# Optimization experiments

Measured on AMD Instinct MI355X. Metric: run time of the kernel, lower is better.

The kernel has to match this reference:

```python
import jax, jax.numpy as jnp
import numpy as np

NUM_NODES = 50000
NUM_EDGES = 1600000
IN_DIM = 128
OUT_DIM = 128
BATCH = 2


def setup_inputs() -> dict:
    key = jax.random.key(0)
    k1, k2, k3 = jax.random.split(key, 3)
    inputs = jax.random.normal(k1, (BATCH, NUM_NODES, IN_DIM), dtype=jnp.float32)
    W = jax.random.normal(k2, (IN_DIM, OUT_DIM), dtype=jnp.float32) * 0.02
    bias = jnp.zeros((1, 1, OUT_DIM), dtype=jnp.float32)
    adjacency_list = jax.random.randint(k3, (NUM_EDGES, 2), 0, NUM_NODES, dtype=jnp.int32)
    return {"inputs": inputs, "W": W, "bias": bias, "adjacency_list": adjacency_list}


def reference(inputs, W, bias, adjacency_list):
    # inputs: (B, N, Din); adjacency_list: (E, 2) with [:,0]=src, [:,1]=dst
    N = inputs.shape[1]
    src = adjacency_list[:, 0]
    dst = adjacency_list[:, 1]
    # symmetric-normalization weights, as computed in __init__
    deg = jnp.bincount(src, length=N)                      # (N,)
    node_w = jnp.sqrt(1.0 / (deg.astype(inputs.dtype) + 1.0))  # (N,)
    edge_w = node_w[src] * node_w[dst]                     # (E,)
    # dense projection (no activation: activation=None)
    x = jnp.einsum('bnd,do->bno', inputs, W)               # (B, N, Dout)
    # gather by edge source, scale by edge weight
    gathered = x[:, src, :] * edge_w[None, :, None]        # (B, E, Dout)
    # scatter-add into destination nodes (unsorted_segment_sum)
    agg = jnp.zeros_like(x).at[:, dst, :].add(gathered)    # (B, N, Dout)
    # self-loop term + aggregated neighbors + bias
    out = (node_w ** 2)[None, :, None] * x + agg + bias
    return out
```

## Files before the change

### kernel.cpp

```cpp
#include <hip/hip_runtime.h>
#include <hip/hip_bf16.h>


#define NN 50000
#define EE 1600000
#define DD 128
#define BB 2
#define NB 128
#define CHUNK 12500
#define HS 50000
#define HW4 (HS / 4)

typedef __attribute__((ext_vector_type(8))) short short8;
typedef __attribute__((ext_vector_type(8))) unsigned short ushort8v;
typedef __attribute__((ext_vector_type(4))) float floatx4;

__device__ inline unsigned short f2bf(float f) {
    unsigned u = __float_as_uint(f);
    unsigned r = u + 0x7fffu + ((u >> 16) & 1u);
    return (unsigned short)(r >> 16);
}
__device__ inline float bf2f(unsigned short h) {
    return __uint_as_float(((unsigned)h) << 16);
}

__global__ __launch_bounds__(1024) void phist_kernel(const int4* __restrict__ adj2,
                                                     unsigned int* __restrict__ histD32,
                                                     unsigned int* __restrict__ histS32,
                                                     unsigned char* __restrict__ rank) {
    __shared__ unsigned int h[HW4];
    int b = blockIdx.x;
    int p0 = b * (CHUNK / 2);

    for (int i = threadIdx.x; i < HW4; i += 1024) h[i] = 0;
    __syncthreads();
    if (blockIdx.y == 0) {
        for (int i = threadIdx.x; i < CHUNK / 2; i += 1024) {
            int4 two = adj2[p0 + i];
            unsigned ka = (unsigned)two.y, kb = (unsigned)two.w;
            unsigned sha = (ka & 3u) << 3, shb = (kb & 3u) << 3;
            unsigned olda = atomicAdd(&h[ka >> 2], 1u << sha);
            unsigned oldb = atomicAdd(&h[kb >> 2], 1u << shb);
            unsigned r0 = (olda >> sha) & 0xffu;
            unsigned r1 = (oldb >> shb) & 0xffu;
            int e = b * CHUNK + 2 * i;
            *(unsigned short*)(rank + e) = (unsigned short)(r0 | (r1 << 8));
        }
        __syncthreads();
        for (int i = threadIdx.x; i < HW4; i += 1024) histD32[(size_t)b * HW4 + i] = h[i];
    } else {
        for (int i = threadIdx.x; i < CHUNK / 2; i += 1024) {
            int4 two = adj2[p0 + i];
            unsigned ka = (unsigned)two.x, kb = (unsigned)two.z;
            atomicAdd(&h[ka >> 2], 1u << ((ka & 3u) << 3));
            atomicAdd(&h[kb >> 2], 1u << ((kb & 3u) << 3));
        }
        __syncthreads();
        for (int i = threadIdx.x; i < HW4; i += 1024) histS32[(size_t)b * HW4 + i] = h[i];
    }
}

__global__ __launch_bounds__(256) void reduce_hist_kernel(unsigned char* __restrict__ histD,
                                                          const unsigned char* __restrict__ histS,
                                                          unsigned char* __restrict__ deg8,
                                                          float* __restrict__ node_w,
                                                          int* __restrict__ blocksum) {
    int k = blockIdx.x * 256 + threadIdx.x;
    unsigned run = 0;
    if (k < NN) {
#pragma unroll 8
        for (int b = 0; b < NB; ++b) {
            size_t idx = (size_t)b * HS + k;
            unsigned c = histD[idx];
            histD[idx] = (unsigned char)run;
            run += c;
        }
        deg8[k] = (unsigned char)run;

        unsigned s = 0;
#pragma unroll 8
        for (int b = 0; b < NB; ++b) s += histS[(size_t)b * HS + k];
        node_w[k] = rsqrtf((float)s + 1.0f);
    }
    __shared__ int red[256];
    red[threadIdx.x] = (int)run;
    __syncthreads();
    for (int s2 = 128; s2 > 0; s2 >>= 1) {
        if (threadIdx.x < s2) red[threadIdx.x] += red[threadIdx.x + s2];
        __syncthreads();
    }
    if (threadIdx.x == 0) blocksum[blockIdx.x] = red[0];
}

__global__ __launch_bounds__(256) void offsets_kernel(const unsigned char* __restrict__ deg8,
                                                      const int* __restrict__ blocksum,
                                                      int* __restrict__ offsets) {
    __shared__ int base_s;
    __shared__ int s[256];
    int bid = blockIdx.x;
    if (threadIdx.x < 64) {
        int v = 0;
        for (int i = threadIdx.x; i < bid; i += 64) v += blocksum[i];
#pragma unroll
        for (int o = 32; o > 0; o >>= 1) v += __shfl_down(v, o);
        if (threadIdx.x == 0) base_s = v;
    }
    int t = bid * 256 + threadIdx.x;
    int d = (t < NN) ? deg8[t] : 0;
    s[threadIdx.x] = d;
    __syncthreads();
    for (int off = 1; off < 256; off <<= 1) {
        int v = (threadIdx.x >= off) ? s[threadIdx.x - off] : 0;
        __syncthreads();
        s[threadIdx.x] += v;
        __syncthreads();
    }
    if (t < NN) offsets[t] = base_s + s[threadIdx.x] - d;
}

__global__ __launch_bounds__(256) void scatter_kernel(const int4* __restrict__ adj2,
                                                      const unsigned short* __restrict__ rank16,
                                                      const unsigned char* __restrict__ histD,
                                                      const int* __restrict__ offsets,
                                                      unsigned short* __restrict__ csr_src) {
    int i = blockIdx.x * blockDim.x + threadIdx.x;
    int4 two = adj2[i];
    unsigned rr = rank16[i];
    int e = 2 * i;
    int b = e / CHUNK;
    int posA = offsets[two.y] + (int)histD[(size_t)b * HS + two.y] + (int)(rr & 0xffu);
    int posB = offsets[two.w] + (int)histD[(size_t)b * HS + two.w] + (int)(rr >> 8);
    csr_src[posA] = (unsigned short)two.x;
    csr_src[posB] = (unsigned short)two.z;
}

#define WT_STRIDE 136
__global__ __launch_bounds__(1024) void gemm_mfma_kernel(const float* __restrict__ in,
                                                         const float* __restrict__ W,
                                                         const float* __restrict__ node_w,
                                                         unsigned short* __restrict__ y,
                                                         int total_rows) {
    __shared__ unsigned short wt[128 * WT_STRIDE];
    for (int i = threadIdx.x; i < 128 * 128; i += 1024) {
        int d = i >> 7, o = i & 127;
        wt[o * WT_STRIDE + d] = f2bf(W[i]);
    }
    __syncthreads();

    int wave = threadIdx.x >> 6;
    int lane = threadIdx.x & 63;
    int m = lane & 15;
    int quad = lane >> 4;
    int rt = (blockIdx.x * 16 + wave) * 16;
    if (rt >= total_rows) return;

    short8 a[4];
    const float* arow = in + (size_t)(rt + m) * 128;
#pragma unroll
    for (int kt = 0; kt < 4; ++kt) {
        int k0 = kt * 32 + quad * 8;
        float4 f0 = *(const float4*)(arow + k0);
        float4 f1 = *(const float4*)(arow + k0 + 4);
        short8 av;
        av[0] = (short)f2bf(f0.x); av[1] = (short)f2bf(f0.y);
        av[2] = (short)f2bf(f0.z); av[3] = (short)f2bf(f0.w);
        av[4] = (short)f2bf(f1.x); av[5] = (short)f2bf(f1.y);
        av[6] = (short)f2bf(f1.z); av[7] = (short)f2bf(f1.w);
        a[kt] = av;
    }

    float nw[4];
#pragma unroll
    for (int r = 0; r < 4; ++r) {
        int row = rt + quad * 4 + r;
        int n = row - (row >= NN ? NN : 0);
        nw[r] = node_w[n];
    }

#pragma unroll
    for (int ct = 0; ct < 8; ++ct) {
        floatx4 acc = {0.f, 0.f, 0.f, 0.f};
#pragma unroll
        for (int kt = 0; kt < 4; ++kt) {
            const short8* bp =
                (const short8*)&wt[(ct * 16 + m) * WT_STRIDE + kt * 32 + quad * 8];
            acc = __builtin_amdgcn_mfma_f32_16x16x32_bf16(a[kt], *bp, acc, 0, 0, 0);
        }
        int col = ct * 16 + m;
#pragma unroll
        for (int r = 0; r < 4; ++r) {
            int row = rt + quad * 4 + r;
            y[(size_t)row * 128 + col] = f2bf(nw[r] * acc[r]);
        }
    }
}

__global__ __launch_bounds__(256) void aggregate_kernel(
    const unsigned short* __restrict__ yb, const unsigned short* __restrict__ csr_src,
    const int* __restrict__ offsets, const unsigned char* __restrict__ deg8,
    const float* __restrict__ node_w, const float* __restrict__ bias,
    float* __restrict__ out) {
    int wave = threadIdx.x >> 6;
    int lane = threadIdx.x & 63;
    unsigned blk = blockIdx.x;
    int xcd = (int)(blk & 7u);
    int bg = xcd >> 2;
    int nbid = (int)(blk >> 3) * 4 + (xcd & 3);
    int n = nbid * 4 + wave;

    int g = lane >> 4;
    int c8 = lane & 15;
    int c16 = c8 * 16;
    const char* ybase = (const char*)yb + (size_t)bg * (NN * 128 * 2);

    int start = offsets[n];
    int cnt = deg8[n];

    float acc[8];
#pragma unroll
    for (int k = 0; k < 8; ++k) acc[k] = 0.f;

    for (int base = 0; base < cnt; base += 64) {
        int mm = cnt - base; if (mm > 64) mm = 64;
        int v = (lane < mm) ? (int)csr_src[start + base + lane] : 0x7fffffff;
#pragma unroll
        for (int k = 2; k <= 64; k <<= 1) {
#pragma unroll
            for (int j = k >> 1; j > 0; j >>= 1) {
                int other = __shfl_xor(v, j);
                bool lower = (lane & j) == 0;
                bool up = (lane & k) == 0;
                int mn = other < v ? other : v;
                int mx = other < v ? v : other;
                v = up ? (lower ? mn : mx) : (lower ? mx : mn);
            }
        }
        int sv = v << 8;
        int j = 0;
        for (; j + 16 <= mm; j += 16) {
            int o0 = __shfl(sv, j + g) + c16;
            int o1 = __shfl(sv, j + 4 + g) + c16;
            int o2 = __shfl(sv, j + 8 + g) + c16;
            int o3 = __shfl(sv, j + 12 + g) + c16;
            ushort8v ld0 = *(const ushort8v*)(ybase + (unsigned)o0);
            ushort8v ld1 = *(const ushort8v*)(ybase + (unsigned)o1);
            ushort8v ld2 = *(const ushort8v*)(ybase + (unsigned)o2);
            ushort8v ld3 = *(const ushort8v*)(ybase + (unsigned)o3);
#pragma unroll
            for (int k = 0; k < 8; ++k) acc[k] += bf2f((unsigned short)ld0[k]);
#pragma unroll
            for (int k = 0; k < 8; ++k) acc[k] += bf2f((unsigned short)ld1[k]);
#pragma unroll
            for (int k = 0; k < 8; ++k) acc[k] += bf2f((unsigned short)ld2[k]);
#pragma unroll
            for (int k = 0; k < 8; ++k) acc[k] += bf2f((unsigned short)ld3[k]);
        }
        for (; j + 8 <= mm; j += 8) {
            int o0 = __shfl(sv, j + g) + c16;
            int o1 = __shfl(sv, j + 4 + g) + c16;
            ushort8v ld0 = *(const ushort8v*)(ybase + (unsigned)o0);
            ushort8v ld1 = *(const ushort8v*)(ybase + (unsigned)o1);
#pragma unroll
            for (int k = 0; k < 8; ++k) acc[k] += bf2f((unsigned short)ld0[k]);
#pragma unroll
            for (int k = 0; k < 8; ++k) acc[k] += bf2f((unsigned short)ld1[k]);
        }
        if (j < mm) {
            int i0 = j + g, i1 = j + 4 + g;
            int o0 = __shfl(sv, i0 < mm ? i0 : 0) + c16;
            int o1 = __shfl(sv, i1 < mm ? i1 : 0) + c16;
            if (i0 < mm) {
                ushort8v ld0 = *(const ushort8v*)(ybase + (unsigned)o0);
#pragma unroll
                for (int k = 0; k < 8; ++k) acc[k] += bf2f((unsigned short)ld0[k]);
            }
            if (i1 < mm) {
                ushort8v ld1 = *(const ushort8v*)(ybase + (unsigned)o1);
#pragma unroll
                for (int k = 0; k < 8; ++k) acc[k] += bf2f((unsigned short)ld1[k]);
            }
        }
    }

#pragma unroll
    for (int k = 0; k < 8; ++k) {
        acc[k] += __shfl_xor(acc[k], 16);
        acc[k] += __shfl_xor(acc[k], 32);
    }

    if (g == 0) {
        float nw = node_w[n];
        const unsigned short* ys = yb + (size_t)bg * (NN * 128) + (size_t)n * 128 + c8 * 8;
        ushort8v yv = *(const ushort8v*)ys;
        floatx4 o0, o1;
        const float* bp = bias + c8 * 8;
        o0.x = nw * (acc[0] + bf2f((unsigned short)yv[0])) + bp[0];
        o0.y = nw * (acc[1] + bf2f((unsigned short)yv[1])) + bp[1];
        o0.z = nw * (acc[2] + bf2f((unsigned short)yv[2])) + bp[2];
        o0.w = nw * (acc[3] + bf2f((unsigned short)yv[3])) + bp[3];
        o1.x = nw * (acc[4] + bf2f((unsigned short)yv[4])) + bp[4];
        o1.y = nw * (acc[5] + bf2f((unsigned short)yv[5])) + bp[5];
        o1.z = nw * (acc[6] + bf2f((unsigned short)yv[6])) + bp[6];
        o1.w = nw * (acc[7] + bf2f((unsigned short)yv[7])) + bp[7];
        float* op = out + ((size_t)bg * NN + n) * 128 + c8 * 8;
        __builtin_nontemporal_store(o0, (floatx4*)op);
        __builtin_nontemporal_store(o1, (floatx4*)(op + 4));
    }
}

extern "C" void kernel_launch(void* const* d_in, const int* in_sizes, int n_in,
                              void* d_out, int out_size, void* d_ws, size_t ws_size,
                              hipStream_t stream) {
    const float* inputs = (const float*)d_in[0];
    const float* W      = (const float*)d_in[1];
    const float* bias   = (const float*)d_in[2];
    const int*   adj    = (const int*)d_in[3];
    float* out = (float*)d_out;

    const int total_rows = BB * NN;

    char* ws = (char*)d_ws;
    size_t off = 0;
    unsigned short* y = (unsigned short*)(ws + off);
    off += (size_t)BB * NN * DD * sizeof(unsigned short);
    unsigned char* histD = (unsigned char*)(ws + off);
    off += (size_t)NB * HS;
    unsigned char* histS = (unsigned char*)(ws + off);
    off += (size_t)NB * HS;
    unsigned short* csr_src = (unsigned short*)histS;
    unsigned char* rank = (unsigned char*)(ws + off);
    off += (size_t)EE;
    unsigned char* deg8 = (unsigned char*)(ws + off);
    off += (size_t)((NN + 255) & ~255);
    float* node_w = (float*)(ws + off);  off += (size_t)NN * sizeof(float);
    int* offsets = (int*)(ws + off);     off += (size_t)NN * sizeof(int);
    int* blocksum = (int*)(ws + off);    off += 256 * sizeof(int);

    dim3 hgrid(NB, 2);
    phist_kernel<<<hgrid, 1024, 0, stream>>>((const int4*)adj, (unsigned int*)histD,
                                             (unsigned int*)histS, rank);
    reduce_hist_kernel<<<(NN + 255) / 256, 256, 0, stream>>>(histD, histS, deg8, node_w,
                                                             blocksum);
    offsets_kernel<<<(NN + 255) / 256, 256, 0, stream>>>(deg8, blocksum, offsets);
    scatter_kernel<<<EE / 2 / 256, 256, 0, stream>>>((const int4*)adj,
                                                     (const unsigned short*)rank, histD, offsets,
                                                     csr_src);
    gemm_mfma_kernel<<<(total_rows + 255) / 256, 1024, 0, stream>>>(inputs, W, node_w, y,
                                                                    total_rows);
    aggregate_kernel<<<NN / 4 * BB, 256, 0, stream>>>(y, csr_src, offsets, deg8, node_w, bias,
                                                      out);
}
```

Before: 265.5 us.

## Fuse CSR scatter and MFMA GEMM into one interleaved kernel launch

Merges the independent edge-scatter and projection GEMM kernels into a single launch. Block indices are interleaved so that every third block does GEMM work and the other two do scatter work, letting the memory-bound scatter overlap with the compute-bound GEMM and removing one launch and its serialization point. Scatter blocks now use 1024 threads and still allocate the GEMM's static shared memory, which can lower occupancy for them. The aggregate kernel also gets an occupancy hint in its launch bounds and readfirstlane on the per-node start and count values to keep them in scalar registers.

```diff
diff --git a/kernel.cpp b/kernel.cpp
--- a/kernel.cpp
+++ b/kernel.cpp
@@ -10,6 +10,9 @@
 #define CHUNK 12500
 #define HS 50000
 #define HW4 (HS / 4)
+
+#define GEMM_BLOCKS 391
+#define SCAT_BLOCKS 782
 
 typedef __attribute__((ext_vector_type(8))) short short8;
 typedef __attribute__((ext_vector_type(8))) unsigned short ushort8v;
@@ -118,28 +121,29 @@
     if (t < NN) offsets[t] = base_s + s[threadIdx.x] - d;
 }
 
-__global__ __launch_bounds__(256) void scatter_kernel(const int4* __restrict__ adj2,
-                                                      const unsigned short* __restrict__ rank16,
-                                                      const unsigned char* __restrict__ histD,
-                                                      const int* __restrict__ offsets,
-                                                      unsigned short* __restrict__ csr_src) {
-    int i = blockIdx.x * blockDim.x + threadIdx.x;
-    int4 two = adj2[i];
-    unsigned rr = rank16[i];
-    int e = 2 * i;
-    int b = e / CHUNK;
-    int posA = offsets[two.y] + (int)histD[(size_t)b * HS + two.y] + (int)(rr & 0xffu);
-    int posB = offsets[two.w] + (int)histD[(size_t)b * HS + two.w] + (int)(rr >> 8);
-    csr_src[posA] = (unsigned short)two.x;
-    csr_src[posB] = (unsigned short)two.z;
-}
-
 #define WT_STRIDE 136
-__global__ __launch_bounds__(1024) void gemm_mfma_kernel(const float* __restrict__ in,
-                                                         const float* __restrict__ W,
-                                                         const float* __restrict__ node_w,
-                                                         unsigned short* __restrict__ y,
-                                                         int total_rows) {
+__global__ __launch_bounds__(1024) void scatter_gemm_kernel(
+    const int4* __restrict__ adj2, const unsigned short* __restrict__ rank16,
+    const unsigned char* __restrict__ histD, const int* __restrict__ offsets,
+    unsigned short* __restrict__ csr_src,
+    const float* __restrict__ in, const float* __restrict__ W,
+    const float* __restrict__ node_w, unsigned short* __restrict__ y) {
+    int bx = blockIdx.x;
+    int gq = bx / 3, r = bx - 3 * gq;
+    if (r != 0) {
+        int i = (2 * gq + r - 1) * 1024 + threadIdx.x;
+        if (i < EE / 2) {
+            int4 two = adj2[i];
+            unsigned rr = rank16[i];
+            int e = 2 * i;
+            int b = e / CHUNK;
+            int posA = offsets[two.y] + (int)histD[(size_t)b * HS + two.y] + (int)(rr & 0xffu);
+            int posB = offsets[two.w] + (int)histD[(size_t)b * HS + two.w] + (int)(rr >> 8);
+            csr_src[posA] = (unsigned short)two.x;
+            csr_src[posB] = (unsigned short)two.z;
+        }
+        return;
+    }
     __shared__ unsigned short wt[128 * WT_STRIDE];
     for (int i = threadIdx.x; i < 128 * 128; i += 1024) {
         int d = i >> 7, o = i & 127;
@@ -151,8 +155,8 @@
     int lane = threadIdx.x & 63;
     int m = lane & 15;
     int quad = lane >> 4;
-    int rt = (blockIdx.x * 16 + wave) * 16;
-    if (rt >= total_rows) return;
+    int rt = (gq * 16 + wave) * 16;
+    if (rt >= BB * NN) return;
 
     short8 a[4];
     const float* arow = in + (size_t)(rt + m) * 128;
@@ -171,10 +175,10 @@
 
     float nw[4];
 #pragma unroll
-    for (int r = 0; r < 4; ++r) {
-        int row = rt + quad * 4 + r;
+    for (int rr = 0; rr < 4; ++rr) {
+        int row = rt + quad * 4 + rr;
         int n = row - (row >= NN ? NN : 0);
-        nw[r] = node_w[n];
+        nw[rr] = node_w[n];
     }
 
 #pragma unroll
@@ -188,14 +192,14 @@
         }
         int col = ct * 16 + m;
 #pragma unroll
-        for (int r = 0; r < 4; ++r) {
-            int row = rt + quad * 4 + r;
-            y[(size_t)row * 128 + col] = f2bf(nw[r] * acc[r]);
-        }
-    }
-}
-
-__global__ __launch_bounds__(256) void aggregate_kernel(
+        for (int rr = 0; rr < 4; ++rr) {
+            int row = rt + quad * 4 + rr;
+            y[(size_t)row * 128 + col] = f2bf(nw[rr] * acc[rr]);
+        }
+    }
+}
+
+__global__ __launch_bounds__(256, 8) void aggregate_kernel(
     const unsigned short* __restrict__ yb, const unsigned short* __restrict__ csr_src,
     const int* __restrict__ offsets, const unsigned char* __restrict__ deg8,
     const float* __restrict__ node_w, const float* __restrict__ bias,
@@ -213,8 +217,8 @@
     int c16 = c8 * 16;
     const char* ybase = (const char*)yb + (size_t)bg * (NN * 128 * 2);
 
-    int start = offsets[n];
-    int cnt = deg8[n];
+    int start = __builtin_amdgcn_readfirstlane(offsets[n]);
+    int cnt = __builtin_amdgcn_readfirstlane((int)deg8[n]);
 
     float acc[8];
 #pragma unroll
@@ -317,8 +321,6 @@
     const int*   adj    = (const int*)d_in[3];
     float* out = (float*)d_out;
 
-    const int total_rows = BB * NN;
-
     char* ws = (char*)d_ws;
     size_t off = 0;
     unsigned short* y = (unsigned short*)(ws + off);
@@ -342,11 +344,9 @@
     reduce_hist_kernel<<<(NN + 255) / 256, 256, 0, stream>>>(histD, histS, deg8, node_w,
                                                              blocksum);
     offsets_kernel<<<(NN + 255) / 256, 256, 0, stream>>>(deg8, blocksum, offsets);
-    scatter_kernel<<<EE / 2 / 256, 256, 0, stream>>>((const int4*)adj,
-                                                     (const unsigned short*)rank, histD, offsets,
-                                                     csr_src);
-    gemm_mfma_kernel<<<(total_rows + 255) / 256, 1024, 0, stream>>>(inputs, W, node_w, y,
-                                                                    total_rows);
+    scatter_gemm_kernel<<<GEMM_BLOCKS + SCAT_BLOCKS, 1024, 0, stream>>>(
+        (const int4*)adj, (const unsigned short*)rank, histD, offsets, csr_src,
+        inputs, W, node_w, y);
     aggregate_kernel<<<NN / 4 * BB, 256, 0, stream>>>(y, csr_src, offsets, deg8, node_w, bias,
                                                       out);
 }
```

Result: no change. 267.9 us (+0.9%).

## Process both batches per wave in aggregate kernel, sharing CSR sort

Applied to the files above, without the earlier changes.

Each wave now handles one node for both batch entries: lanes 0-31 work on batch 0 and lanes 32-63 on batch 1. The CSR neighbor loads and the bitonic sort are shared, which halves the grid and removes the duplicated index work. The old XCD-aware block remapping is gone, so L2 locality of the gathered y rows across XCDs may suffer. The change also adds wave-uniform readfirstlane for start/count and a launch_bounds occupancy hint of 8 blocks.

```diff
diff --git a/kernel.cpp b/kernel.cpp
--- a/kernel.cpp
+++ b/kernel.cpp
@@ -195,26 +195,23 @@
     }
 }
 
-__global__ __launch_bounds__(256) void aggregate_kernel(
+__global__ __launch_bounds__(256, 8) void aggregate_kernel(
     const unsigned short* __restrict__ yb, const unsigned short* __restrict__ csr_src,
     const int* __restrict__ offsets, const unsigned char* __restrict__ deg8,
     const float* __restrict__ node_w, const float* __restrict__ bias,
     float* __restrict__ out) {
     int wave = threadIdx.x >> 6;
     int lane = threadIdx.x & 63;
-    unsigned blk = blockIdx.x;
-    int xcd = (int)(blk & 7u);
-    int bg = xcd >> 2;
-    int nbid = (int)(blk >> 3) * 4 + (xcd & 3);
-    int n = nbid * 4 + wave;
-
-    int g = lane >> 4;
+    int n = blockIdx.x * 4 + wave;
+
+    int b32 = lane >> 5;
+    int g = (lane >> 4) & 1;
     int c8 = lane & 15;
     int c16 = c8 * 16;
-    const char* ybase = (const char*)yb + (size_t)bg * (NN * 128 * 2);
-
-    int start = offsets[n];
-    int cnt = deg8[n];
+    const char* ybase = (const char*)yb + (size_t)b32 * (NN * 128 * 2);
+
+    int start = __builtin_amdgcn_readfirstlane(offsets[n]);
+    int cnt = __builtin_amdgcn_readfirstlane((int)deg8[n]);
 
     float acc[8];
 #pragma unroll
@@ -237,11 +234,11 @@
         }
         int sv = v << 8;
         int j = 0;
-        for (; j + 16 <= mm; j += 16) {
+        for (; j + 8 <= mm; j += 8) {
             int o0 = __shfl(sv, j + g) + c16;
-            int o1 = __shfl(sv, j + 4 + g) + c16;
-            int o2 = __shfl(sv, j + 8 + g) + c16;
-            int o3 = __shfl(sv, j + 12 + g) + c16;
+            int o1 = __shfl(sv, j + 2 + g) + c16;
+            int o2 = __shfl(sv, j + 4 + g) + c16;
+            int o3 = __shfl(sv, j + 6 + g) + c16;
             ushort8v ld0 = *(const ushort8v*)(ybase + (unsigned)o0);
             ushort8v ld1 = *(const ushort8v*)(ybase + (unsigned)o1);
             ushort8v ld2 = *(const ushort8v*)(ybase + (unsigned)o2);
@@ -255,9 +252,9 @@
 #pragma unroll
             for (int k = 0; k < 8; ++k) acc[k] += bf2f((unsigned short)ld3[k]);
         }
-        for (; j + 8 <= mm; j += 8) {
+        for (; j + 4 <= mm; j += 4) {
             int o0 = __shfl(sv, j + g) + c16;
-            int o1 = __shfl(sv, j + 4 + g) + c16;
+            int o1 = __shfl(sv, j + 2 + g) + c16;
             ushort8v ld0 = *(const ushort8v*)(ybase + (unsigned)o0);
             ushort8v ld1 = *(const ushort8v*)(ybase + (unsigned)o1);
 #pragma unroll
@@ -265,32 +262,31 @@
 #pragma unroll
             for (int k = 0; k < 8; ++k) acc[k] += bf2f((unsigned short)ld1[k]);
         }
+        if (j + 2 <= mm) {
+            int o0 = __shfl(sv, j + g) + c16;
+            ushort8v ld0 = *(const ushort8v*)(ybase + (unsigned)o0);
+#pragma unroll
+            for (int k = 0; k < 8; ++k) acc[k] += bf2f((unsigned short)ld0[k]);
+            j += 2;
+        }
         if (j < mm) {
-            int i0 = j + g, i1 = j + 4 + g;
+            int i0 = j + g;
             int o0 = __shfl(sv, i0 < mm ? i0 : 0) + c16;
-            int o1 = __shfl(sv, i1 < mm ? i1 : 0) + c16;
             if (i0 < mm) {
                 ushort8v ld0 = *(const ushort8v*)(ybase + (unsigned)o0);
 #pragma unroll
                 for (int k = 0; k < 8; ++k) acc[k] += bf2f((unsigned short)ld0[k]);
             }
-            if (i1 < mm) {
-                ushort8v ld1 = *(const ushort8v*)(ybase + (unsigned)o1);
-#pragma unroll
-                for (int k = 0; k < 8; ++k) acc[k] += bf2f((unsigned short)ld1[k]);
-            }
-        }
-    }
-
-#pragma unroll
-    for (int k = 0; k < 8; ++k) {
-        acc[k] += __shfl_xor(acc[k], 16);
-        acc[k] += __shfl_xor(acc[k], 32);
-    }
+        }
+    }
+
+#pragma unroll
+    for (int k = 0; k < 8; ++k) acc[k] += __shfl_xor(acc[k], 16);
 
     if (g == 0) {
         float nw = node_w[n];
-        const unsigned short* ys = yb + (size_t)bg * (NN * 128) + (size_t)n * 128 + c8 * 8;
+        const unsigned short* ys =
+            yb + (size_t)b32 * (NN * 128) + (size_t)n * 128 + c8 * 8;
         ushort8v yv = *(const ushort8v*)ys;
         floatx4 o0, o1;
         const float* bp = bias + c8 * 8;
@@ -302,7 +298,7 @@
         o1.y = nw * (acc[5] + bf2f((unsigned short)yv[5])) + bp[5];
         o1.z = nw * (acc[6] + bf2f((unsigned short)yv[6])) + bp[6];
         o1.w = nw * (acc[7] + bf2f((unsigned short)yv[7])) + bp[7];
-        float* op = out + ((size_t)bg * NN + n) * 128 + c8 * 8;
+        float* op = out + ((size_t)b32 * NN + n) * 128 + c8 * 8;
         __builtin_nontemporal_store(o0, (floatx4*)op);
         __builtin_nontemporal_store(o1, (floatx4*)(op + 4));
     }
@@ -347,6 +343,6 @@
                                                      csr_src);
     gemm_mfma_kernel<<<(total_rows + 255) / 256, 1024, 0, stream>>>(inputs, W, node_w, y,
                                                                     total_rows);
-    aggregate_kernel<<<NN / 4 * BB, 256, 0, stream>>>(y, csr_src, offsets, deg8, node_w, bias,
-                                                      out);
-}
+    aggregate_kernel<<<NN / 4, 256, 0, stream>>>(y, csr_src, offsets, deg8, node_w, bias,
+                                                 out);
+}
```

Result: slower. 273.1 us (+2.8%).
